# Performance work log

Hardware: AMD Instinct MI355X
Metric: run time of the kernel (lower is better)

The kernel has to match this reference:

```python
import jax, jax.numpy as jnp
import numpy as np

H = 12  # num_heads

def _attn(q, k, v):
    # q,k,v: [B,H,N,D]; SDPA default scale 1/sqrt(D)
    D = q.shape[-1]
    scores = jnp.einsum('bhnd,bhmd->bhnm', q, k) / jnp.sqrt(jnp.asarray(D, q.dtype))
    p = jax.nn.softmax(scores, axis=-1)
    return jnp.einsum('bhnm,bhmd->bhnd', p, v)

def setup_inputs() -> dict:
    key = jax.random.key(0)
    ks = jax.random.split(key, 5)
    B, N, C = 2, 2048, 768
    s = 0.02
    return {
        'x': jax.random.normal(ks[0], (B, N, C), jnp.float32),
        'Wq': jax.random.normal(ks[1], (C, 2 * C), jnp.float32) * s,
        'Wk': jax.random.normal(ks[2], (C, 2 * C), jnp.float32) * s,
        'Wv': jax.random.normal(ks[3], (C, C), jnp.float32) * s,
        'lambda_p': jnp.zeros((H, 1, 1), jnp.float32),
        'Wo': jax.random.normal(ks[4], (C, C), jnp.float32) * s,
        'bo': jnp.zeros((C,), jnp.float32),
    }

def reference(x, Wq, Wk, Wv, lambda_p, Wo, bo):
    B, N, C = x.shape
    D = C // H
    # [B,N,2C] -> [2,B,H,N,D]
    q = (x @ Wq).reshape(B, N, 2, H, D).transpose(2, 0, 3, 1, 4)
    k = (x @ Wk).reshape(B, N, 2, H, D).transpose(2, 0, 3, 1, 4)
    v = (x @ Wv).reshape(B, N, H, D).transpose(0, 2, 1, 3)
    out1 = _attn(q[0], k[0], v)
    out2 = _attn(q[1], k[1], v)
    lam = jnp.exp(lambda_p)  # [H,1,1] broadcasts over [B,H,N,D]
    out = out1 - lam * out2
    out = out.transpose(0, 2, 1, 3).reshape(B, N, C)
    return out @ Wo + bo
```

## Files before the change

### kernel.cpp

```cpp
#include <hip/hip_runtime.h>

typedef unsigned short u16;
typedef unsigned int u32;
typedef unsigned long long u64;
typedef __bf16 bf16x8 __attribute__((ext_vector_type(8)));
typedef float f32x4 __attribute__((ext_vector_type(4)));

#define B_ 2
#define N_ 2048
#define C_ 768
#define H_ 12
#define M_ 4096

static __device__ __forceinline__ u16 f2bf(float f) {
  u32 u = __builtin_bit_cast(u32, f);
  u32 r = u + 0x7fffu + ((u >> 16) & 1u);
  return (u16)(r >> 16);
}
static __device__ __forceinline__ float bf2f(u16 h) {
  u32 u = ((u32)h) << 16;
  return __builtin_bit_cast(float, u);
}
static __device__ __forceinline__ float fexp2(float x) {
#if __has_builtin(__builtin_amdgcn_exp2f)
  return __builtin_amdgcn_exp2f(x);
#else
  return __expf(x * 0.6931471805599453f);
#endif
}
static __device__ __forceinline__ u32 pack_bf16(float a, float b) {
  u32 r;
  asm("v_cvt_pk_bf16_f32 %0, %1, %2" : "=v"(r) : "v"(a), "v"(b));
  return r;
}

static __device__ __forceinline__ void gload16(const void* g, void* lds_base) {
  __builtin_amdgcn_global_load_lds(
      (__attribute__((address_space(1))) void*)(u64)(g),
      (__attribute__((address_space(3))) void*)(u32)(u64)(lds_base), 16, 0, 0);
}

__global__ __launch_bounds__(256) void k_cvt4(const float* __restrict__ x,
                                              u16* __restrict__ xb, int n4) {
  int i = blockIdx.x * 256 + threadIdx.x;
  if (i >= n4) return;
  float4 v = ((const float4*)x)[i];
  ushort4 o;
  o.x = f2bf(v.x); o.y = f2bf(v.y); o.z = f2bf(v.z); o.w = f2bf(v.w);
  ((ushort4*)xb)[i] = o;
}

__global__ __launch_bounds__(256) void k_tconv2(const float* __restrict__ W0,
                                                const float* __restrict__ W1,
                                                u16* __restrict__ Wt, int K, int N) {
  const float* W = blockIdx.z ? W1 : W0;
  u16* dst = Wt + (u64)blockIdx.z * N * K;
  __shared__ float t[32][33];
  int n0 = blockIdx.x * 32, k0 = blockIdx.y * 32;
  int tx = threadIdx.x, ty = threadIdx.y;
#pragma unroll
  for (int i = 0; i < 4; i++)
    t[ty + i * 8][tx] = W[(u64)(k0 + ty + i * 8) * N + n0 + tx];
  __syncthreads();
#pragma unroll
  for (int i = 0; i < 4; i++)
    dst[(u64)(n0 + ty + i * 8) * K + k0 + tx] = f2bf(t[tx][ty + i * 8]);
}

template <int EPI>
__global__ __launch_bounds__(256) void k_gemm(const u16* __restrict__ A,
                                              const u16* __restrict__ Bt,
                                              void* __restrict__ Cout,
                                              const float* __restrict__ bias,
                                              int Msz, int Nsz, int Ksz) {
  __shared__ u16 As[128 * 32];
  __shared__ u16 Bs[128 * 32];
  const int t = threadIdx.x;
  const int w = t >> 6, l = t & 63;
  const int wr = w >> 1, wc = w & 1;
  const int la = l & 15, lg = l >> 4;
  const int srow = l >> 2, scb = (l & 3) << 4;

  f32x4 acc[4][4];
#pragma unroll
  for (int i = 0; i < 4; i++)
#pragma unroll
    for (int j = 0; j < 4; j++) acc[i][j] = f32x4{0.f, 0.f, 0.f, 0.f};

  const u16* Ag = A + (u64)(blockIdx.x * 128) * Ksz;
  const u16* Bg = Bt + (u64)(blockIdx.y * 128) * Ksz;

  for (int k0 = 0; k0 < Ksz; k0 += 32) {
#pragma unroll
    for (int j = 0; j < 2; j++) {
      int r = (w * 2 + j) * 16 + srow;
      gload16((const char*)(Ag + (u64)r * Ksz + k0) + scb,
              (char*)As + (w * 2 + j) * 1024);
      gload16((const char*)(Bg + (u64)r * Ksz + k0) + scb,
              (char*)Bs + (w * 2 + j) * 1024);
    }
    __syncthreads();
    bf16x8 af[4], bfr[4];
#pragma unroll
    for (int m = 0; m < 4; m++)
      af[m] = *(const bf16x8*)(As + (wr * 64 + m * 16 + la) * 32 + lg * 8);
#pragma unroll
    for (int n = 0; n < 4; n++)
      bfr[n] = *(const bf16x8*)(Bs + (wc * 64 + n * 16 + la) * 32 + lg * 8);
#pragma unroll
    for (int m = 0; m < 4; m++)
#pragma unroll
      for (int n = 0; n < 4; n++)
        acc[m][n] =
            __builtin_amdgcn_mfma_f32_16x16x32_bf16(af[m], bfr[n], acc[m][n], 0, 0, 0);
    __syncthreads();
  }

#pragma unroll
  for (int m = 0; m < 4; m++) {
#pragma unroll
    for (int n = 0; n < 4; n++) {
      int grow0 = blockIdx.x * 128 + wr * 64 + m * 16 + lg * 4;
      int gcol = blockIdx.y * 128 + wc * 64 + n * 16 + la;
      if (EPI == 0) {
        u16* Cp = (u16*)Cout;
#pragma unroll
        for (int j = 0; j < 4; j++)
          Cp[(u64)(grow0 + j) * Nsz + gcol] = f2bf(acc[m][n][j]);
      } else if (EPI == 1) {
        u16* Cp = (u16*)Cout;
        ushort4 o;
        o.x = f2bf(acc[m][n][0]); o.y = f2bf(acc[m][n][1]);
        o.z = f2bf(acc[m][n][2]); o.w = f2bf(acc[m][n][3]);
        *(ushort4*)(Cp + (u64)gcol * Msz + grow0) = o;
      } else {
        float* Cp = (float*)Cout;
        float bb = bias[gcol];
#pragma unroll
        for (int j = 0; j < 4; j++)
          Cp[(u64)(grow0 + j) * Nsz + gcol] = acc[m][n][j] + bb;
      }
    }
  }
}

__global__ __launch_bounds__(256, 3) void k_attn2(const u16* __restrict__ QKb,
                                                  const u16* __restrict__ Vt,
                                                  const float* __restrict__ lamp,
                                                  u16* __restrict__ Ob) {
  const int qt = blockIdx.x, h = blockIdx.y, b = blockIdx.z;
  __shared__ u16 Ks[2][4096];
  __shared__ u16 Vs[4096];
  __shared__ u16 Ps[4][1024];
  const int t = threadIdx.x, w = t >> 6, l = t & 63;
  const int la = l & 15, lg = l >> 4;

  const u16* qrow =
      QKb + (u64)(b * N_ + qt * 64 + w * 16 + la) * 3072 + h * 64 + lg * 8;
  bf16x8 qf00 = *(const bf16x8*)(qrow);
  bf16x8 qf01 = *(const bf16x8*)(qrow + 32);
  bf16x8 qf10 = *(const bf16x8*)(qrow + 768);
  bf16x8 qf11 = *(const bf16x8*)(qrow + 800);

  f32x4 oacc[2][4];
#pragma unroll
  for (int p = 0; p < 2; p++)
#pragma unroll
    for (int i = 0; i < 4; i++) oacc[p][i] = f32x4{0.f, 0.f, 0.f, 0.f};
  float m_run[2] = {-1e30f, -1e30f}, l_run[2] = {0.f, 0.f};

  const int rA = t >> 3, cb = (t & 7) << 4;
  const u32 swA = (u32)(rA * 128 + (cb ^ ((rA & 7) << 4)));
  const char* kg = (const char*)(QKb + (u64)(b * N_ + rA) * 3072 + 1536 + h * 64) + cb;
  const char* vg = (const char*)(Vt + (u64)(h * 64 + rA) * M_ + b * N_) + cb;
  const u64 KR32 = (u64)32 * 3072 * 2;
  const u64 VR32 = (u64)32 * M_ * 2;
  const u64 KSTEP = (u64)64 * 3072 * 2;

  uint4 rk0A, rk0B, rk1A, rk1B, rvA, rvB;
#define ATTN_LOADS()                             \
  do {                                           \
    rk0A = *(const uint4*)(kg);                  \
    rk0B = *(const uint4*)(kg + KR32);           \
    rk1A = *(const uint4*)(kg + 1536);           \
    rk1B = *(const uint4*)(kg + 1536 + KR32);    \
    rvA = *(const uint4*)(vg);                   \
    rvB = *(const uint4*)(vg + VR32);            \
  } while (0)

  ATTN_LOADS();

  char* ks0 = (char*)Ks[0];
  char* ks1 = (char*)Ks[1];
  char* vsp = (char*)Vs;
  char* pw = (char*)Ps[w];
  const int sw2 = (la & 7) << 4;
  const float SCALE = 0.18033688f;

  for (int kt = 0; kt < 32; kt++) {
    asm volatile("s_waitcnt vmcnt(0)" ::: "memory");
    __builtin_amdgcn_sched_barrier(0);
    *(uint4*)(ks0 + swA) = rk0A;
    *(uint4*)(ks0 + swA + 4096) = rk0B;
    *(uint4*)(ks1 + swA) = rk1A;
    *(uint4*)(ks1 + swA + 4096) = rk1B;
    *(uint4*)(vsp + swA) = rvA;
    *(uint4*)(vsp + swA + 4096) = rvB;
    asm volatile("s_waitcnt lgkmcnt(0)" ::: "memory");
    __builtin_amdgcn_s_barrier();
    kg += KSTEP;
    vg += 128;
    if (kt < 31) ATTN_LOADS();
    __builtin_amdgcn_sched_barrier(0);

#pragma unroll
    for (int p = 0; p < 2; p++) {
      const char* ksp = p ? ks1 : ks0;
      bf16x8 q0 = p ? qf10 : qf00;
      bf16x8 q1 = p ? qf11 : qf01;
      f32x4 st[4];
#pragma unroll
      for (int c = 0; c < 4; c++) {
        int row = c * 16 + la;
        int sw = (row & 7) << 4;
        bf16x8 kf0 = *(const bf16x8*)(ksp + row * 128 + ((lg * 16) ^ sw));
        bf16x8 kf1 = *(const bf16x8*)(ksp + row * 128 + ((64 + lg * 16) ^ sw));
        f32x4 z = f32x4{0.f, 0.f, 0.f, 0.f};
        z = __builtin_amdgcn_mfma_f32_16x16x32_bf16(kf0, q0, z, 0, 0, 0);
        z = __builtin_amdgcn_mfma_f32_16x16x32_bf16(kf1, q1, z, 0, 0, 0);
        st[c] = z * SCALE;
      }
      float pmax = -1e30f;
#pragma unroll
      for (int c = 0; c < 4; c++)
#pragma unroll
        for (int j = 0; j < 4; j++) pmax = fmaxf(pmax, st[c][j]);
      pmax = fmaxf(pmax, __shfl_xor(pmax, 16, 64));
      pmax = fmaxf(pmax, __shfl_xor(pmax, 32, 64));
      float mr = m_run[p];
      if (__any(pmax - mr > 8.f)) {
        float mnew = fmaxf(mr, pmax);
        float corr = fexp2(mr - mnew);
        l_run[p] *= corr;
        float cT0 = __shfl(corr, lg * 4 + 0, 64);
        float cT1 = __shfl(corr, lg * 4 + 1, 64);
        float cT2 = __shfl(corr, lg * 4 + 2, 64);
        float cT3 = __shfl(corr, lg * 4 + 3, 64);
#pragma unroll
        for (int cd = 0; cd < 4; cd++) {
          oacc[p][cd][0] *= cT0;
          oacc[p][cd][1] *= cT1;
          oacc[p][cd][2] *= cT2;
          oacc[p][cd][3] *= cT3;
        }
        m_run[p] = mnew;
        mr = mnew;
      }
      float ls = 0.f;
#pragma unroll
      for (int c = 0; c < 4; c++)
#pragma unroll
        for (int j = 0; j < 4; j++) {
          float e = fexp2(st[c][j] - mr);
          st[c][j] = e;
          ls += e;
        }
      ls += __shfl_xor(ls, 16, 64);
      ls += __shfl_xor(ls, 32, 64);
      l_run[p] += ls;
#pragma unroll
      for (int c = 0; c < 4; c++) {
        u32 lo = pack_bf16(st[c][0], st[c][1]);
        u32 hi = pack_bf16(st[c][2], st[c][3]);
        int kvb = c * 32 + lg * 8;
        *(u32*)(pw + la * 128 + (kvb ^ sw2)) = lo;
        *(u32*)(pw + la * 128 + ((kvb + 4) ^ sw2)) = hi;
      }
      bf16x8 pf0 = *(const bf16x8*)(pw + la * 128 + ((lg * 16) ^ sw2));
      bf16x8 pf1 = *(const bf16x8*)(pw + la * 128 + ((64 + lg * 16) ^ sw2));
#pragma unroll
      for (int cd = 0; cd < 4; cd++) {
        int row = cd * 16 + la;
        int sw = (row & 7) << 4;
        bf16x8 v0 = *(const bf16x8*)(vsp + row * 128 + ((lg * 16) ^ sw));
        bf16x8 v1 = *(const bf16x8*)(vsp + row * 128 + ((64 + lg * 16) ^ sw));
        oacc[p][cd] =
            __builtin_amdgcn_mfma_f32_16x16x32_bf16(pf0, v0, oacc[p][cd], 0, 0, 0);
        oacc[p][cd] =
            __builtin_amdgcn_mfma_f32_16x16x32_bf16(pf1, v1, oacc[p][cd], 0, 0, 0);
      }
    }
    __builtin_amdgcn_s_barrier();
  }

  float lam = __expf(lamp[h]);
  float i0 = 1.f / l_run[0];
  float i1 = 1.f / l_run[1];
  float s0[4], s1[4];
#pragma unroll
  for (int j = 0; j < 4; j++) {
    s0[j] = __shfl(i0, lg * 4 + j, 64);
    s1[j] = __shfl(i1, lg * 4 + j, 64);
  }
  u16* Og = Ob + (u64)(b * N_ + qt * 64 + w * 16) * C_ + h * 64;
#pragma unroll
  for (int cd = 0; cd < 4; cd++) {
    int dcol = cd * 16 + la;
#pragma unroll
    for (int j = 0; j < 4; j++) {
      float v = oacc[0][cd][j] * s0[j] - lam * (oacc[1][cd][j] * s1[j]);
      Og[(u64)(lg * 4 + j) * C_ + dcol] = f2bf(v);
    }
  }
}

extern "C" void kernel_launch(void* const* d_in, const int* in_sizes, int n_in,
                              void* d_out, int out_size, void* d_ws, size_t ws_size,
                              hipStream_t stream) {
  const float* x = (const float*)d_in[0];
  const float* Wq = (const float*)d_in[1];
  const float* Wk = (const float*)d_in[2];
  const float* Wv = (const float*)d_in[3];
  const float* lamp = (const float*)d_in[4];
  const float* Wo = (const float*)d_in[5];
  const float* bo = (const float*)d_in[6];

  char* ws = (char*)d_ws;
  u16* xb = (u16*)ws;    ws += (u64)M_ * C_ * 2;
  u16* wqkt = (u16*)ws;  ws += (u64)4 * C_ * C_ * 2;
  u16* wvo = (u16*)ws;   ws += (u64)2 * C_ * C_ * 2;
  u16* QKb = (u16*)ws;   ws += (u64)M_ * 4 * C_ * 2;
  u16* Vt = (u16*)ws;    ws += (u64)C_ * M_ * 2;
  u16* Ob = (u16*)ws;    ws += (u64)M_ * C_ * 2;
  u16* wvt = wvo;
  u16* wot = wvo + (u64)C_ * C_;

  k_cvt4<<<dim3(M_ * C_ / 4 / 256), 256, 0, stream>>>(x, xb, M_ * C_ / 4);
  k_tconv2<<<dim3(48, 24, 2), dim3(32, 8), 0, stream>>>(Wq, Wk, wqkt, 768, 1536);
  k_tconv2<<<dim3(24, 24, 2), dim3(32, 8), 0, stream>>>(Wv, Wo, wvo, 768, 768);
  k_gemm<0><<<dim3(32, 24), 256, 0, stream>>>(xb, wqkt, QKb, nullptr, M_, 3072, 768);
  k_gemm<1><<<dim3(32, 6), 256, 0, stream>>>(xb, wvt, Vt, nullptr, M_, 768, 768);
  k_attn2<<<dim3(32, 12, 2), 256, 0, stream>>>(QKb, Vt, lamp, Ob);
  k_gemm<2><<<dim3(32, 6), 256, 0, stream>>>(Ob, wot, d_out, bo, M_, 768, 768);
}
```

Baseline: 166.8 us.

## Split differential attention branches across waves and merge QKV GEMMs

The attention kernel moves to 512-thread blocks in which waves 0-3 handle the first softmax branch and waves 4-7 the second, sharing K/V tiles in LDS. The two outputs are combined through shared memory at the end. This doubles wave-level parallelism and lowers per-wave register pressure. The Q and V projection GEMMs are fused into one launch, the softmax scale is folded into the Q epilogue, and the row max uses v_max3. The cost is an extra LDS combine step and a larger block, which may reduce per-CU occupancy flexibility.

Result: faster. 154.5 us (-7.4%).

```diff
diff --git a/kernel.cpp b/kernel.cpp
--- a/kernel.cpp
+++ b/kernel.cpp
@@ -11,15 +11,12 @@
 #define C_ 768
 #define H_ 12
 #define M_ 4096
+#define SCALE_LOG2 0.18033688011112042f
 
 static __device__ __forceinline__ u16 f2bf(float f) {
   u32 u = __builtin_bit_cast(u32, f);
   u32 r = u + 0x7fffu + ((u >> 16) & 1u);
   return (u16)(r >> 16);
-}
-static __device__ __forceinline__ float bf2f(u16 h) {
-  u32 u = ((u32)h) << 16;
-  return __builtin_bit_cast(float, u);
 }
 static __device__ __forceinline__ float fexp2(float x) {
 #if __has_builtin(__builtin_amdgcn_exp2f)
@@ -31,6 +28,11 @@
 static __device__ __forceinline__ u32 pack_bf16(float a, float b) {
   u32 r;
   asm("v_cvt_pk_bf16_f32 %0, %1, %2" : "=v"(r) : "v"(a), "v"(b));
+  return r;
+}
+static __device__ __forceinline__ float max3f(float a, float b, float c) {
+  float r;
+  asm("v_max3_f32 %0, %1, %2, %3" : "=v"(r) : "v"(a), "v"(b), "v"(c));
   return r;
 }
 
@@ -67,12 +69,11 @@
     dst[(u64)(n0 + ty + i * 8) * K + k0 + tx] = f2bf(t[tx][ty + i * 8]);
 }
 
-template <int EPI>
-__global__ __launch_bounds__(256) void k_gemm(const u16* __restrict__ A,
-                                              const u16* __restrict__ Bt,
-                                              void* __restrict__ Cout,
-                                              const float* __restrict__ bias,
-                                              int Msz, int Nsz, int Ksz) {
+__global__ __launch_bounds__(256) void k_gemm_qkv(const u16* __restrict__ A,
+                                                  const u16* __restrict__ WQK,
+                                                  const u16* __restrict__ WV,
+                                                  u16* __restrict__ QKb,
+                                                  u16* __restrict__ Vtout) {
   __shared__ u16 As[128 * 32];
   __shared__ u16 Bs[128 * 32];
   const int t = threadIdx.x;
@@ -80,6 +81,8 @@
   const int wr = w >> 1, wc = w & 1;
   const int la = l & 15, lg = l >> 4;
   const int srow = l >> 2, scb = (l & 3) << 4;
+  const int by = blockIdx.y;
+  const bool isV = by >= 24;
 
   f32x4 acc[4][4];
 #pragma unroll
@@ -87,17 +90,15 @@
 #pragma unroll
     for (int j = 0; j < 4; j++) acc[i][j] = f32x4{0.f, 0.f, 0.f, 0.f};
 
-  const u16* Ag = A + (u64)(blockIdx.x * 128) * Ksz;
-  const u16* Bg = Bt + (u64)(blockIdx.y * 128) * Ksz;
-
-  for (int k0 = 0; k0 < Ksz; k0 += 32) {
+  const u16* Ag = A + (u64)(blockIdx.x * 128) * 768;
+  const u16* Bg = isV ? WV + (u64)((by - 24) * 128) * 768 : WQK + (u64)(by * 128) * 768;
+
+  for (int k0 = 0; k0 < 768; k0 += 32) {
 #pragma unroll
     for (int j = 0; j < 2; j++) {
       int r = (w * 2 + j) * 16 + srow;
-      gload16((const char*)(Ag + (u64)r * Ksz + k0) + scb,
-              (char*)As + (w * 2 + j) * 1024);
-      gload16((const char*)(Bg + (u64)r * Ksz + k0) + scb,
-              (char*)Bs + (w * 2 + j) * 1024);
+      gload16((const char*)(Ag + (u64)r * 768 + k0) + scb, (char*)As + (w * 2 + j) * 1024);
+      gload16((const char*)(Bg + (u64)r * 768 + k0) + scb, (char*)Bs + (w * 2 + j) * 1024);
     }
     __syncthreads();
     bf16x8 af[4], bfr[4];
@@ -121,196 +122,234 @@
 #pragma unroll
     for (int n = 0; n < 4; n++) {
       int grow0 = blockIdx.x * 128 + wr * 64 + m * 16 + lg * 4;
-      int gcol = blockIdx.y * 128 + wc * 64 + n * 16 + la;
-      if (EPI == 0) {
-        u16* Cp = (u16*)Cout;
+      if (!isV) {
+        int gcol = by * 128 + wc * 64 + n * 16 + la;
+        float sc = (gcol < 1536) ? SCALE_LOG2 : 1.0f;
 #pragma unroll
         for (int j = 0; j < 4; j++)
-          Cp[(u64)(grow0 + j) * Nsz + gcol] = f2bf(acc[m][n][j]);
-      } else if (EPI == 1) {
-        u16* Cp = (u16*)Cout;
+          QKb[(u64)(grow0 + j) * 3072 + gcol] = f2bf(acc[m][n][j] * sc);
+      } else {
+        int gcol = (by - 24) * 128 + wc * 64 + n * 16 + la;
         ushort4 o;
         o.x = f2bf(acc[m][n][0]); o.y = f2bf(acc[m][n][1]);
         o.z = f2bf(acc[m][n][2]); o.w = f2bf(acc[m][n][3]);
-        *(ushort4*)(Cp + (u64)gcol * Msz + grow0) = o;
-      } else {
-        float* Cp = (float*)Cout;
-        float bb = bias[gcol];
-#pragma unroll
-        for (int j = 0; j < 4; j++)
-          Cp[(u64)(grow0 + j) * Nsz + gcol] = acc[m][n][j] + bb;
+        *(ushort4*)(Vtout + (u64)gcol * M_ + grow0) = o;
       }
     }
   }
 }
 
-__global__ __launch_bounds__(256, 3) void k_attn2(const u16* __restrict__ QKb,
+__global__ __launch_bounds__(256) void k_gemm_out(const u16* __restrict__ A,
+                                                  const u16* __restrict__ Bt,
+                                                  float* __restrict__ Cout,
+                                                  const float* __restrict__ bias) {
+  __shared__ u16 As[128 * 32];
+  __shared__ u16 Bs[128 * 32];
+  const int t = threadIdx.x;
+  const int w = t >> 6, l = t & 63;
+  const int wr = w >> 1, wc = w & 1;
+  const int la = l & 15, lg = l >> 4;
+  const int srow = l >> 2, scb = (l & 3) << 4;
+
+  f32x4 acc[4][4];
+#pragma unroll
+  for (int i = 0; i < 4; i++)
+#pragma unroll
+    for (int j = 0; j < 4; j++) acc[i][j] = f32x4{0.f, 0.f, 0.f, 0.f};
+
+  const u16* Ag = A + (u64)(blockIdx.x * 128) * 768;
+  const u16* Bg = Bt + (u64)(blockIdx.y * 128) * 768;
+
+  for (int k0 = 0; k0 < 768; k0 += 32) {
+#pragma unroll
+    for (int j = 0; j < 2; j++) {
+      int r = (w * 2 + j) * 16 + srow;
+      gload16((const char*)(Ag + (u64)r * 768 + k0) + scb, (char*)As + (w * 2 + j) * 1024);
+      gload16((const char*)(Bg + (u64)r * 768 + k0) + scb, (char*)Bs + (w * 2 + j) * 1024);
+    }
+    __syncthreads();
+    bf16x8 af[4], bfr[4];
+#pragma unroll
+    for (int m = 0; m < 4; m++)
+      af[m] = *(const bf16x8*)(As + (wr * 64 + m * 16 + la) * 32 + lg * 8);
+#pragma unroll
+    for (int n = 0; n < 4; n++)
+      bfr[n] = *(const bf16x8*)(Bs + (wc * 64 + n * 16 + la) * 32 + lg * 8);
+#pragma unroll
+    for (int m = 0; m < 4; m++)
+#pragma unroll
+      for (int n = 0; n < 4; n++)
+        acc[m][n] =
+            __builtin_amdgcn_mfma_f32_16x16x32_bf16(af[m], bfr[n], acc[m][n], 0, 0, 0);
+    __syncthreads();
+  }
+
+#pragma unroll
+  for (int m = 0; m < 4; m++) {
+#pragma unroll
+    for (int n = 0; n < 4; n++) {
+      int grow0 = blockIdx.x * 128 + wr * 64 + m * 16 + lg * 4;
+      int gcol = blockIdx.y * 128 + wc * 64 + n * 16 + la;
+      float bb = bias[gcol];
+#pragma unroll
+      for (int j = 0; j < 4; j++)
+        Cout[(u64)(grow0 + j) * 768 + gcol] = acc[m][n][j] + bb;
+    }
+  }
+}
+
+__global__ __launch_bounds__(512, 6) void k_attn3(const u16* __restrict__ QKb,
                                                   const u16* __restrict__ Vt,
                                                   const float* __restrict__ lamp,
                                                   u16* __restrict__ Ob) {
   const int qt = blockIdx.x, h = blockIdx.y, b = blockIdx.z;
-  __shared__ u16 Ks[2][4096];
-  __shared__ u16 Vs[4096];
-  __shared__ u16 Ps[4][1024];
+  __shared__ __align__(16) char smem[40960];
+  char* ks0 = smem;
+  char* ks1 = smem + 8192;
+  char* vsp = smem + 16384;
   const int t = threadIdx.x, w = t >> 6, l = t & 63;
+  const int p = w >> 2, wq = w & 3;
+  char* pw = smem + 24576 + w * 2048;
   const int la = l & 15, lg = l >> 4;
+  const int sw2 = (la & 7) << 4;
 
   const u16* qrow =
-      QKb + (u64)(b * N_ + qt * 64 + w * 16 + la) * 3072 + h * 64 + lg * 8;
-  bf16x8 qf00 = *(const bf16x8*)(qrow);
-  bf16x8 qf01 = *(const bf16x8*)(qrow + 32);
-  bf16x8 qf10 = *(const bf16x8*)(qrow + 768);
-  bf16x8 qf11 = *(const bf16x8*)(qrow + 800);
-
-  f32x4 oacc[2][4];
-#pragma unroll
-  for (int p = 0; p < 2; p++)
-#pragma unroll
-    for (int i = 0; i < 4; i++) oacc[p][i] = f32x4{0.f, 0.f, 0.f, 0.f};
-  float m_run[2] = {-1e30f, -1e30f}, l_run[2] = {0.f, 0.f};
-
-  const int rA = t >> 3, cb = (t & 7) << 4;
-  const u32 swA = (u32)(rA * 128 + (cb ^ ((rA & 7) << 4)));
-  const char* kg = (const char*)(QKb + (u64)(b * N_ + rA) * 3072 + 1536 + h * 64) + cb;
-  const char* vg = (const char*)(Vt + (u64)(h * 64 + rA) * M_ + b * N_) + cb;
-  const u64 KR32 = (u64)32 * 3072 * 2;
-  const u64 VR32 = (u64)32 * M_ * 2;
+      QKb + (u64)(b * N_ + qt * 64 + wq * 16 + la) * 3072 + p * 768 + h * 64 + lg * 8;
+  bf16x8 q0 = *(const bf16x8*)(qrow);
+  bf16x8 q1 = *(const bf16x8*)(qrow + 32);
+
+  f32x4 oacc[4];
+#pragma unroll
+  for (int i = 0; i < 4; i++) oacc[i] = f32x4{0.f, 0.f, 0.f, 0.f};
+  float m_run = -1e30f, l_run = 0.f;
+
+  const int rA = t >> 3, cbs = (t & 7) << 4;
+  const u32 swA = (u32)(rA * 128 + (cbs ^ ((rA & 7) << 4)));
+  const char* kg = (const char*)(QKb + (u64)(b * N_ + rA) * 3072 + 1536 + h * 64) + cbs;
+  const char* vg = (const char*)(Vt + (u64)(h * 64 + rA) * M_ + b * N_) + cbs;
   const u64 KSTEP = (u64)64 * 3072 * 2;
 
-  uint4 rk0A, rk0B, rk1A, rk1B, rvA, rvB;
-#define ATTN_LOADS()                             \
-  do {                                           \
-    rk0A = *(const uint4*)(kg);                  \
-    rk0B = *(const uint4*)(kg + KR32);           \
-    rk1A = *(const uint4*)(kg + 1536);           \
-    rk1B = *(const uint4*)(kg + 1536 + KR32);    \
-    rvA = *(const uint4*)(vg);                   \
-    rvB = *(const uint4*)(vg + VR32);            \
-  } while (0)
-
-  ATTN_LOADS();
-
-  char* ks0 = (char*)Ks[0];
-  char* ks1 = (char*)Ks[1];
-  char* vsp = (char*)Vs;
-  char* pw = (char*)Ps[w];
-  const int sw2 = (la & 7) << 4;
-  const float SCALE = 0.18033688f;
+  uint4 rk0, rk1, rv;
+  rk0 = *(const uint4*)(kg);
+  rk1 = *(const uint4*)(kg + 1536);
+  rv = *(const uint4*)(vg);
+
+  const char* ksp = p ? ks1 : ks0;
 
   for (int kt = 0; kt < 32; kt++) {
     asm volatile("s_waitcnt vmcnt(0)" ::: "memory");
     __builtin_amdgcn_sched_barrier(0);
-    *(uint4*)(ks0 + swA) = rk0A;
-    *(uint4*)(ks0 + swA + 4096) = rk0B;
-    *(uint4*)(ks1 + swA) = rk1A;
-    *(uint4*)(ks1 + swA + 4096) = rk1B;
-    *(uint4*)(vsp + swA) = rvA;
-    *(uint4*)(vsp + swA + 4096) = rvB;
+    *(uint4*)(ks0 + swA) = rk0;
+    *(uint4*)(ks1 + swA) = rk1;
+    *(uint4*)(vsp + swA) = rv;
     asm volatile("s_waitcnt lgkmcnt(0)" ::: "memory");
     __builtin_amdgcn_s_barrier();
     kg += KSTEP;
     vg += 128;
-    if (kt < 31) ATTN_LOADS();
+    if (kt < 31) {
+      rk0 = *(const uint4*)(kg);
+      rk1 = *(const uint4*)(kg + 1536);
+      rv = *(const uint4*)(vg);
+    }
     __builtin_amdgcn_sched_barrier(0);
 
-#pragma unroll
-    for (int p = 0; p < 2; p++) {
-      const char* ksp = p ? ks1 : ks0;
-      bf16x8 q0 = p ? qf10 : qf00;
-      bf16x8 q1 = p ? qf11 : qf01;
-      f32x4 st[4];
-#pragma unroll
-      for (int c = 0; c < 4; c++) {
-        int row = c * 16 + la;
-        int sw = (row & 7) << 4;
-        bf16x8 kf0 = *(const bf16x8*)(ksp + row * 128 + ((lg * 16) ^ sw));
-        bf16x8 kf1 = *(const bf16x8*)(ksp + row * 128 + ((64 + lg * 16) ^ sw));
-        f32x4 z = f32x4{0.f, 0.f, 0.f, 0.f};
-        z = __builtin_amdgcn_mfma_f32_16x16x32_bf16(kf0, q0, z, 0, 0, 0);
-        z = __builtin_amdgcn_mfma_f32_16x16x32_bf16(kf1, q1, z, 0, 0, 0);
-        st[c] = z * SCALE;
+    f32x4 st[4];
+#pragma unroll
+    for (int c = 0; c < 4; c++) {
+      int row = c * 16 + la;
+      int sw = (row & 7) << 4;
+      bf16x8 kf0 = *(const bf16x8*)(ksp + row * 128 + ((lg * 16) ^ sw));
+      bf16x8 kf1 = *(const bf16x8*)(ksp + row * 128 + ((64 + lg * 16) ^ sw));
+      f32x4 z = f32x4{0.f, 0.f, 0.f, 0.f};
+      z = __builtin_amdgcn_mfma_f32_16x16x32_bf16(kf0, q0, z, 0, 0, 0);
+      z = __builtin_amdgcn_mfma_f32_16x16x32_bf16(kf1, q1, z, 0, 0, 0);
+      st[c] = z;
+    }
+    float m0 = max3f(st[0][0], st[0][1], st[0][2]);
+    float m1 = max3f(st[0][3], st[1][0], st[1][1]);
+    float m2 = max3f(st[1][2], st[1][3], st[2][0]);
+    float m3 = max3f(st[2][1], st[2][2], st[2][3]);
+    float m4 = max3f(st[3][0], st[3][1], st[3][2]);
+    float pmax = fmaxf(max3f(m0, m1, m2), max3f(m3, m4, st[3][3]));
+    pmax = fmaxf(pmax, __shfl_xor(pmax, 16, 64));
+    pmax = fmaxf(pmax, __shfl_xor(pmax, 32, 64));
+    if (__any(pmax - m_run > 8.f)) {
+      float mnew = fmaxf(m_run, pmax);
+      float corr = fexp2(m_run - mnew);
+      l_run *= corr;
+      float cT0 = __shfl(corr, lg * 4 + 0, 64);
+      float cT1 = __shfl(corr, lg * 4 + 1, 64);
+      float cT2 = __shfl(corr, lg * 4 + 2, 64);
+      float cT3 = __shfl(corr, lg * 4 + 3, 64);
+#pragma unroll
+      for (int cd = 0; cd < 4; cd++) {
+        oacc[cd][0] *= cT0;
+        oacc[cd][1] *= cT1;
+        oacc[cd][2] *= cT2;
+        oacc[cd][3] *= cT3;
       }
-      float pmax = -1e30f;
-#pragma unroll
-      for (int c = 0; c < 4; c++)
-#pragma unroll
-        for (int j = 0; j < 4; j++) pmax = fmaxf(pmax, st[c][j]);
-      pmax = fmaxf(pmax, __shfl_xor(pmax, 16, 64));
-      pmax = fmaxf(pmax, __shfl_xor(pmax, 32, 64));
-      float mr = m_run[p];
-      if (__any(pmax - mr > 8.f)) {
-        float mnew = fmaxf(mr, pmax);
-        float corr = fexp2(mr - mnew);
-        l_run[p] *= corr;
-        float cT0 = __shfl(corr, lg * 4 + 0, 64);
-        float cT1 = __shfl(corr, lg * 4 + 1, 64);
-        float cT2 = __shfl(corr, lg * 4 + 2, 64);
-        float cT3 = __shfl(corr, lg * 4 + 3, 64);
-#pragma unroll
-        for (int cd = 0; cd < 4; cd++) {
-          oacc[p][cd][0] *= cT0;
-          oacc[p][cd][1] *= cT1;
-          oacc[p][cd][2] *= cT2;
-          oacc[p][cd][3] *= cT3;
-        }
-        m_run[p] = mnew;
-        mr = mnew;
+      m_run = mnew;
+    }
+    float ls = 0.f;
+#pragma unroll
+    for (int c = 0; c < 4; c++)
+#pragma unroll
+      for (int j = 0; j < 4; j++) {
+        float e = fexp2(st[c][j] - m_run);
+        st[c][j] = e;
+        ls += e;
       }
-      float ls = 0.f;
-#pragma unroll
-      for (int c = 0; c < 4; c++)
-#pragma unroll
-        for (int j = 0; j < 4; j++) {
-          float e = fexp2(st[c][j] - mr);
-          st[c][j] = e;
-          ls += e;
-        }
-      ls += __shfl_xor(ls, 16, 64);
-      ls += __shfl_xor(ls, 32, 64);
-      l_run[p] += ls;
-#pragma unroll
-      for (int c = 0; c < 4; c++) {
-        u32 lo = pack_bf16(st[c][0], st[c][1]);
-        u32 hi = pack_bf16(st[c][2], st[c][3]);
-        int kvb = c * 32 + lg * 8;
-        *(u32*)(pw + la * 128 + (kvb ^ sw2)) = lo;
-        *(u32*)(pw + la * 128 + ((kvb + 4) ^ sw2)) = hi;
+    ls += __shfl_xor(ls, 16, 64);
+    ls += __shfl_xor(ls, 32, 64);
+    l_run += ls;
+#pragma unroll
+    for (int c = 0; c < 4; c++) {
+      uint2 pr;
+      pr.x = pack_bf16(st[c][0], st[c][1]);
+      pr.y = pack_bf16(st[c][2], st[c][3]);
+      int kvb = c * 32 + lg * 8;
+      *(uint2*)(pw + la * 128 + (kvb ^ sw2)) = pr;
+    }
+    bf16x8 pf0 = *(const bf16x8*)(pw + la * 128 + ((lg * 16) ^ sw2));
+    bf16x8 pf1 = *(const bf16x8*)(pw + la * 128 + ((64 + lg * 16) ^ sw2));
+#pragma unroll
+    for (int cd = 0; cd < 4; cd++) {
+      int row = cd * 16 + la;
+      int sw = (row & 7) << 4;
+      bf16x8 v0 = *(const bf16x8*)(vsp + row * 128 + ((lg * 16) ^ sw));
+      bf16x8 v1 = *(const bf16x8*)(vsp + row * 128 + ((64 + lg * 16) ^ sw));
+      oacc[cd] = __builtin_amdgcn_mfma_f32_16x16x32_bf16(pf0, v0, oacc[cd], 0, 0, 0);
+      oacc[cd] = __builtin_amdgcn_mfma_f32_16x16x32_bf16(pf1, v1, oacc[cd], 0, 0, 0);
+    }
+    __builtin_amdgcn_s_barrier();
+  }
+
+  float inv = 1.f / l_run;
+  float s0 = __shfl(inv, lg * 4 + 0, 64);
+  float s1 = __shfl(inv, lg * 4 + 1, 64);
+  float s2 = __shfl(inv, lg * 4 + 2, 64);
+  float s3 = __shfl(inv, lg * 4 + 3, 64);
+  float sj[4] = {s0, s1, s2, s3};
+  float* cmb = (float*)smem + wq * (16 * 66);
+  __syncthreads();
+  if (p == 1) {
+    float lam = __expf(lamp[h]);
+#pragma unroll
+    for (int cd = 0; cd < 4; cd++)
+#pragma unroll
+      for (int j = 0; j < 4; j++)
+        cmb[(lg * 4 + j) * 66 + cd * 16 + la] = lam * oacc[cd][j] * sj[j];
+  }
+  __syncthreads();
+  if (p == 0) {
+    u16* Og = Ob + (u64)(b * N_ + qt * 64 + wq * 16) * C_ + h * 64;
+#pragma unroll
+    for (int cd = 0; cd < 4; cd++)
+#pragma unroll
+      for (int j = 0; j < 4; j++) {
+        float v = oacc[cd][j] * sj[j] - cmb[(lg * 4 + j) * 66 + cd * 16 + la];
+        Og[(u64)(lg * 4 + j) * C_ + cd * 16 + la] = f2bf(v);
       }
-      bf16x8 pf0 = *(const bf16x8*)(pw + la * 128 + ((lg * 16) ^ sw2));
-      bf16x8 pf1 = *(const bf16x8*)(pw + la * 128 + ((64 + lg * 16) ^ sw2));
-#pragma unroll
-      for (int cd = 0; cd < 4; cd++) {
-        int row = cd * 16 + la;
-        int sw = (row & 7) << 4;
-        bf16x8 v0 = *(const bf16x8*)(vsp + row * 128 + ((lg * 16) ^ sw));
-        bf16x8 v1 = *(const bf16x8*)(vsp + row * 128 + ((64 + lg * 16) ^ sw));
-        oacc[p][cd] =
-            __builtin_amdgcn_mfma_f32_16x16x32_bf16(pf0, v0, oacc[p][cd], 0, 0, 0);
-        oacc[p][cd] =
-            __builtin_amdgcn_mfma_f32_16x16x32_bf16(pf1, v1, oacc[p][cd], 0, 0, 0);
-      }
-    }
-    __builtin_amdgcn_s_barrier();
-  }
-
-  float lam = __expf(lamp[h]);
-  float i0 = 1.f / l_run[0];
-  float i1 = 1.f / l_run[1];
-  float s0[4], s1[4];
-#pragma unroll
-  for (int j = 0; j < 4; j++) {
-    s0[j] = __shfl(i0, lg * 4 + j, 64);
-    s1[j] = __shfl(i1, lg * 4 + j, 64);
-  }
-  u16* Og = Ob + (u64)(b * N_ + qt * 64 + w * 16) * C_ + h * 64;
-#pragma unroll
-  for (int cd = 0; cd < 4; cd++) {
-    int dcol = cd * 16 + la;
-#pragma unroll
-    for (int j = 0; j < 4; j++) {
-      float v = oacc[0][cd][j] * s0[j] - lam * (oacc[1][cd][j] * s1[j]);
-      Og[(u64)(lg * 4 + j) * C_ + dcol] = f2bf(v);
-    }
   }
 }
 
@@ -338,8 +377,7 @@
   k_cvt4<<<dim3(M_ * C_ / 4 / 256), 256, 0, stream>>>(x, xb, M_ * C_ / 4);
   k_tconv2<<<dim3(48, 24, 2), dim3(32, 8), 0, stream>>>(Wq, Wk, wqkt, 768, 1536);
   k_tconv2<<<dim3(24, 24, 2), dim3(32, 8), 0, stream>>>(Wv, Wo, wvo, 768, 768);
-  k_gemm<0><<<dim3(32, 24), 256, 0, stream>>>(xb, wqkt, QKb, nullptr, M_, 3072, 768);
-  k_gemm<1><<<dim3(32, 6), 256, 0, stream>>>(xb, wvt, Vt, nullptr, M_, 768, 768);
-  k_attn2<<<dim3(32, 12, 2), 256, 0, stream>>>(QKb, Vt, lamp, Ob);
-  k_gemm<2><<<dim3(32, 6), 256, 0, stream>>>(Ob, wot, d_out, bo, M_, 768, 768);
-}
+  k_gemm_qkv<<<dim3(32, 30), 256, 0, stream>>>(xb, wqkt, wvt, QKb, Vt);
+  k_attn3<<<dim3(32, 12, 2), 512, 0, stream>>>(QKb, Vt, lamp, Ob);
+  k_gemm_out<<<dim3(32, 6), 256, 0, stream>>>(Ob, wot, (float*)d_out, bo);
+}
```
